# Optimization experiments

Measured on AMD Instinct MI355X. Metric: run time of the kernel, lower is better.

## Reference

```python
import jax, jax.numpy as jnp
import numpy as np

B, T, D, Uh = 64, 512, 1024, 1024

def _uniform(key, shape, scale=0.05):
    return jax.random.uniform(key, shape, dtype=jnp.float32, minval=-scale, maxval=scale)

def setup_inputs() -> dict:
    key = jax.random.key(0)
    ks = jax.random.split(key, 15)
    inp = {"x": jax.random.normal(ks[0], (B, T, D), dtype=jnp.float32)}
    names = ["fw", "fu", "fb", "iw", "iu", "ib", "cw", "cu", "cb", "ow", "ou", "ob"]
    shapes = [(D, Uh), (Uh, Uh), (Uh,)] * 4
    for n, s, k in zip(names, shapes, ks[1:13]):
        inp[n] = _uniform(k, s)
    inp["h0"] = _uniform(ks[13], (1, Uh))
    return inp

def reference(x, fw, fu, fb, iw, iu, ib, cw, cu, cb, ow, ou, ob, h0):
    # Concatenate the 4 gate weight matrices along the output dim: (D, 4U), (U, 4U), (4U,)
    W = jnp.concatenate([fw, iw, cw, ow], axis=1)
    Umat = jnp.concatenate([fu, iu, cu, ou], axis=1)
    b = jnp.concatenate([fb, ib, cb, ob], axis=0)
    # Input-to-gate projections for all timesteps at once: (B, T, 4U)
    xw = jnp.einsum('btd,dg->btg', x, W) + b
    h_init = jnp.repeat(h0, x.shape[0], axis=0)  # (B, U)

    def step(h, xw_t):
        g = xw_t + h @ Umat  # (B, 4U)
        f, i, c, o = jnp.split(g, 4, axis=-1)
        h1 = jax.nn.sigmoid(f) * h + jax.nn.sigmoid(i) * jnp.tanh(c)
        y1 = jax.nn.sigmoid(o) * jnp.tanh(h1)
        return h1, y1

    _, ys = jax.lax.scan(step, h_init, jnp.swapaxes(xw, 0, 1))  # ys: (T, B, U)
    return jnp.swapaxes(ys, 0, 1)  # (B, T, U)
```

## Files before the change

kernel.cpp:

```cpp
#include <hip/hip_runtime.h>
#include <hip/hip_bf16.h>

#define BB 64
#define TT 512
#define DD 1024
#define UU 1024

typedef __attribute__((ext_vector_type(8))) short short8;
typedef __attribute__((ext_vector_type(4))) float f32x4;
typedef unsigned long long ull;

static __device__ __forceinline__ unsigned short f2bf(float f) {
    unsigned int u = __float_as_uint(f);
    unsigned int r = (u + 0x7fffu + ((u >> 16) & 1u)) >> 16;
    return (unsigned short)r;
}
static __device__ __forceinline__ float bf2f(unsigned short s) {
    return __uint_as_float(((unsigned int)s) << 16);
}
static __device__ __forceinline__ float fsig(float x) {
    return 1.0f / (1.0f + __expf(-x));
}
static __device__ __forceinline__ float ftanh(float x) {
    float e = __expf(-2.0f * fabsf(x));
    float r = (1.0f - e) / (1.0f + e);
    return __builtin_copysignf(r, x);
}

__global__ __launch_bounds__(256) void pack_w(
    const float* __restrict__ w0, const float* __restrict__ w1,
    const float* __restrict__ w2, const float* __restrict__ w3,
    short* __restrict__ out)
{
    int tid = blockIdx.x * 256 + threadIdx.x;
    int lane = tid & 63;
    int kb = (tid >> 6) & 31;
    int n16 = tid >> 11;
    int col = (n16 << 4) + (lane & 15);
    int g = col >> 10, u = col & 1023;
    const float* __restrict__ src = (g == 0) ? w0 : (g == 1) ? w1 : (g == 2) ? w2 : w3;
    int kbase = kb * 32 + ((lane >> 4) << 3);
    short8 p;
#pragma unroll
    for (int i = 0; i < 8; ++i) p[i] = (short)f2bf(src[(size_t)(kbase + i) * UU + u]);
    *reinterpret_cast<short8*>(out + (size_t)tid * 8) = p;
}

__global__ __launch_bounds__(256) void init_hbf(const float* __restrict__ h0,
                                                unsigned short* __restrict__ hb)
{
    int i = blockIdx.x * 256 + threadIdx.x;
    hb[i] = f2bf(h0[i & (UU - 1)]);
}

__global__ __launch_bounds__(256) void gemm_xw(
    const float* __restrict__ x, const short* __restrict__ wpk,
    const float* __restrict__ fb, const float* __restrict__ ib,
    const float* __restrict__ cb, const float* __restrict__ ob,
    unsigned short* __restrict__ xw)
{
    __shared__ short As[128 * 40];
    __shared__ short Bs[8 * 512];

    const int tid = threadIdx.x;
    const int lane = tid & 63;
    const int wid = tid >> 6;
    const int wr = wid >> 1, wc = wid & 1;
    const int n0 = blockIdx.x << 7;
    const int m0 = blockIdx.y << 7;
    const int n16b = n0 >> 4;

    const int srow = tid >> 1;
    const int kh = tid & 1;
    const float* __restrict__ xrow = x + (size_t)(m0 + srow) * DD + kh * 16;
    const short* __restrict__ wsrc =
        wpk + ((size_t)(n16b + (tid >> 5)) * 32) * 512 + (size_t)(tid & 31) * 16;

    f32x4 acc[4][4];
#pragma unroll
    for (int i = 0; i < 4; ++i)
#pragma unroll
        for (int j = 0; j < 4; ++j) acc[i][j] = (f32x4){0.f, 0.f, 0.f, 0.f};

    const int aoff = (wr * 64 + (lane & 15)) * 40 + (lane >> 4) * 8;
    const int boff = (wc * 4) * 512 + lane * 8;

    for (int kb = 0; kb < 32; ++kb) {
        const float4* xp = reinterpret_cast<const float4*>(xrow + kb * 32);
        float4 v0 = xp[0], v1 = xp[1], v2 = xp[2], v3 = xp[3];
        short8 p0, p1;
        p0[0] = (short)f2bf(v0.x); p0[1] = (short)f2bf(v0.y);
        p0[2] = (short)f2bf(v0.z); p0[3] = (short)f2bf(v0.w);
        p0[4] = (short)f2bf(v1.x); p0[5] = (short)f2bf(v1.y);
        p0[6] = (short)f2bf(v1.z); p0[7] = (short)f2bf(v1.w);
        p1[0] = (short)f2bf(v2.x); p1[1] = (short)f2bf(v2.y);
        p1[2] = (short)f2bf(v2.z); p1[3] = (short)f2bf(v2.w);
        p1[4] = (short)f2bf(v3.x); p1[5] = (short)f2bf(v3.y);
        p1[6] = (short)f2bf(v3.z); p1[7] = (short)f2bf(v3.w);
        *reinterpret_cast<short8*>(&As[srow * 40 + kh * 16]) = p0;
        *reinterpret_cast<short8*>(&As[srow * 40 + kh * 16 + 8]) = p1;

        const short8* ws8 = reinterpret_cast<const short8*>(wsrc + (size_t)kb * 512);
        short8 b0v = ws8[0], b1v = ws8[1];
        *reinterpret_cast<short8*>(&Bs[tid * 16]) = b0v;
        *reinterpret_cast<short8*>(&Bs[tid * 16 + 8]) = b1v;
        __syncthreads();

        short8 af[4], bfr[4];
#pragma unroll
        for (int fi = 0; fi < 4; ++fi)
            af[fi] = *reinterpret_cast<const short8*>(&As[aoff + fi * 640]);
#pragma unroll
        for (int fj = 0; fj < 4; ++fj)
            bfr[fj] = *reinterpret_cast<const short8*>(&Bs[boff + fj * 512]);
#pragma unroll
        for (int fi = 0; fi < 4; ++fi)
#pragma unroll
            for (int fj = 0; fj < 4; ++fj)
                acc[fi][fj] = __builtin_amdgcn_mfma_f32_16x16x32_bf16(
                    af[fi], bfr[fj], acc[fi][fj], 0, 0, 0);
        __syncthreads();
    }

    const int g = n0 >> 10;
    const float* __restrict__ bias = (g == 0) ? fb : (g == 1) ? ib : (g == 2) ? cb : ob;
#pragma unroll
    for (int fi = 0; fi < 4; ++fi) {
#pragma unroll
        for (int fj = 0; fj < 4; ++fj) {
            int n = n0 + wc * 64 + fj * 16 + (lane & 15);
            int uc = n & 1023;
            int ub = uc >> 4, ul = uc & 15;
            float bv = bias[uc];
#pragma unroll
            for (int r = 0; r < 4; ++r) {
                int row = m0 + wr * 64 + fi * 16 + (lane >> 4) * 4 + r;
                int b = row >> 9, t = row & 511;
                float v = acc[fi][fj][r] + bv;
                size_t off = (((size_t)t * 64 + ub) * BB + b) * 64 + g * 16 + ul;
                xw[off] = f2bf(v);
            }
        }
    }
}

#define PHASE(MZ, R0, HLS, GBUF, HOWN, OMZ, OHLS, DO_POLL, POLL_T)                 \
  do {                                                                             \
    const unsigned short* __restrict__ xp =                                        \
        xw + ((size_t)t * 64 + ub) * 4096 + (size_t)((R0) + trow) * 64 + tcol;     \
    float xv0 = bf2f(xp[0]);                                                       \
    float xv1 = bf2f(xp[16]);                                                      \
    float xv2 = bf2f(xp[32]);                                                      \
    float xv3 = bf2f(xp[48]);                                                      \
    f32x4 acc0 = (f32x4){0.f, 0.f, 0.f, 0.f};                                      \
    f32x4 acc1 = (f32x4){0.f, 0.f, 0.f, 0.f};                                      \
    _Pragma("unroll")                                                              \
    for (int kg = 0; kg < 32; kg += 2) {                                           \
      short8 a0 = *reinterpret_cast<const short8*>(&HLS[aoff + kg * 32]);          \
      short8 a1 = *reinterpret_cast<const short8*>(&HLS[aoff + kg * 32 + 32]);     \
      acc0 = __builtin_amdgcn_mfma_f32_16x16x32_bf16(a0, bfr[kg], acc0, 0, 0, 0);  \
      acc1 = __builtin_amdgcn_mfma_f32_16x16x32_bf16(a1, bfr[kg + 1], acc1,        \
                                                     0, 0, 0);                     \
    }                                                                              \
    acc0[0] += acc1[0]; acc0[1] += acc1[1];                                        \
    acc0[2] += acc1[2]; acc0[3] += acc1[3];                                        \
    _Pragma("unroll")                                                              \
    for (int r = 0; r < 4; ++r)                                                    \
      GBUF[gi][(lane >> 4) * 4 + r][lane & 15] = acc0[r];                          \
    if (gi == 1 && (DO_POLL)) {                                                    \
      const int* fl = flg + ((size_t)(POLL_T) * 4 + (OMZ)) * 64 + lane;            \
      int v;                                                                       \
      do {                                                                         \
        v = __hip_atomic_load(fl, __ATOMIC_RELAXED, __HIP_MEMORY_SCOPE_AGENT);     \
        if (v == 0) __builtin_amdgcn_s_sleep(1);                                   \
      } while (v == 0);                                                            \
      asm volatile("" ::: "memory");                                               \
      const unsigned short* hc = hrot + (size_t)(POLL_T) * (BB * UU)               \
                                 + ((size_t)(OMZ) << 4) * UU + (size_t)(v - 1);    \
      _Pragma("unroll")                                                            \
      for (int p = 0; p < 32; ++p) {                                               \
        int row = p >> 1, half = p & 1;                                            \
        __builtin_amdgcn_global_load_lds(                                          \
            (const void*)(hc + (size_t)row * 1024 + half * 512 + (size_t)lane * 8),\
            (void*)&OHLS[row * 1032 + half * 512], 16, 0, 16);                     \
      }                                                                            \
    }                                                                              \
    asm volatile("s_waitcnt lgkmcnt(0)" ::: "memory");                             \
    __builtin_amdgcn_s_barrier();                                                  \
    asm volatile("" ::: "memory");                                                 \
    {                                                                              \
      float gf  = GBUF[0][trow][tcol] + xv0;                                       \
      float gii = GBUF[1][trow][tcol] + xv1;                                       \
      float gc  = GBUF[2][trow][tcol] + xv2;                                       \
      float go  = GBUF[3][trow][tcol] + xv3;                                       \
      float h1  = fsig(gf) * (HOWN) + fsig(gii) * ftanh(gc);                       \
      (HOWN) = h1;                                                                 \
      y[((size_t)((R0) + trow) * TT + t) * UU + u0 + tcol] = fsig(go) * ftanh(h1); \
      unsigned int hb16 = f2bf(h1);                                                \
      unsigned int n1 = __shfl_down(hb16, 1);                                      \
      unsigned int n2 = __shfl_down(hb16, 2);                                      \
      unsigned int n3 = __shfl_down(hb16, 3);                                      \
      if (t < TT - 1 && (lane & 3) == 0) {                                         \
        unsigned long long pv =                                                    \
            (unsigned long long)(hb16 | (n1 << 16)) |                              \
            ((unsigned long long)(n2 | (n3 << 16)) << 32);                         \
        unsigned short* dst = hrot + (size_t)(t + 1) * (BB * UU)                   \
                              + (size_t)((R0) + trow) * UU + u0 + tcol;            \
        __hip_atomic_store(reinterpret_cast<ull*>(dst), pv,                        \
                           __ATOMIC_RELAXED, __HIP_MEMORY_SCOPE_AGENT);            \
      }                                                                            \
    }                                                                              \
    __syncthreads();               \
    if (t < TT - 1 && gi == 0 && lane == 0)                                        \
      __hip_atomic_store(flg + ((size_t)(t + 1) * 4 + (MZ)) * 64 + ub, 1,          \
                         __ATOMIC_RELAXED, __HIP_MEMORY_SCOPE_AGENT);              \
  } while (0)

__global__ __launch_bounds__(256, 1) void lstm_scan(
    const unsigned short* __restrict__ xw, const float* __restrict__ h0,
    unsigned short* __restrict__ hrot,
    const short* __restrict__ upk,
    float* __restrict__ y, int* __restrict__ flg)
{
    __shared__ unsigned short hlsA[16 * 1032 + 8];
    __shared__ unsigned short hlsB[16 * 1032 + 8];
    __shared__ float gbufA[4][16][20];
    __shared__ float gbufB[4][16][20];

    const int tid = threadIdx.x;
    const int lane = tid & 63;
    const int gi = tid >> 6;
    const int z  = blockIdx.x >> 6;
    const int ub = blockIdx.x & 63;
    const int mzA = z * 2, mzB = z * 2 + 1;
    const int r0A = mzA << 4, r0B = mzB << 4;
    const int u0 = ub << 4;

    const short* __restrict__ bsrc =
        upk + ((size_t)(gi * 64 + ub) * 32) * 512 + (size_t)lane * 8;
    short8 bfr[32];
#pragma unroll
    for (int kb = 0; kb < 32; ++kb)
        bfr[kb] = *reinterpret_cast<const short8*>(bsrc + (size_t)kb * 512);

    const int aoff = (lane & 15) * 1032 + (lane >> 4) * 8;
    const int trow = tid >> 4, tcol = tid & 15;

    float h_ownA = h0[u0 + tcol];
    float h_ownB = h_ownA;

    if (gi == 1) {
#pragma unroll
        for (int p = 0; p < 32; ++p) {
            int row = p >> 1, half = p & 1;
            __builtin_amdgcn_global_load_lds(
                (const void*)(hrot + (size_t)r0A * UU + (size_t)row * 1024
                              + half * 512 + (size_t)lane * 8),
                (void*)&hlsA[row * 1032 + half * 512], 16, 0, 16);
            __builtin_amdgcn_global_load_lds(
                (const void*)(hrot + (size_t)r0B * UU + (size_t)row * 1024
                              + half * 512 + (size_t)lane * 8),
                (void*)&hlsB[row * 1032 + half * 512], 16, 0, 16);
        }
    }
    __syncthreads();

    for (int t = 0; t < TT; ++t) {
        PHASE(mzA, r0A, hlsA, gbufA, h_ownA, mzB, hlsB, (t >= 1), t);
        PHASE(mzB, r0B, hlsB, gbufB, h_ownB, mzA, hlsA, (t + 1 < TT), t + 1);
    }
}

extern "C" void kernel_launch(void* const* d_in, const int* in_sizes, int n_in,
                              void* d_out, int out_size, void* d_ws, size_t ws_size,
                              hipStream_t stream)
{
    const float* x  = (const float*)d_in[0];
    const float* fw = (const float*)d_in[1];
    const float* fu = (const float*)d_in[2];
    const float* fb = (const float*)d_in[3];
    const float* iw = (const float*)d_in[4];
    const float* iu = (const float*)d_in[5];
    const float* ib = (const float*)d_in[6];
    const float* cw = (const float*)d_in[7];
    const float* cu = (const float*)d_in[8];
    const float* cb = (const float*)d_in[9];
    const float* ow = (const float*)d_in[10];
    const float* ou = (const float*)d_in[11];
    const float* ob = (const float*)d_in[12];
    const float* h0 = (const float*)d_in[13];
    float* y = (float*)d_out;

    const size_t xw_elems = (size_t)TT * BB * 4 * UU;
    const size_t pk_elems = (size_t)4 * 1024 * 1024;
    const size_t hrot_elems = (size_t)(TT + 1) * BB * UU;

    char* wsb = (char*)d_ws;
    unsigned short* xw = (unsigned short*)wsb;
    short* upk = (short*)(wsb + xw_elems * 2);
    short* wpk = upk + pk_elems;
    unsigned short* hrot = (unsigned short*)(wpk + pk_elems);
    int* flg = (int*)(hrot + hrot_elems);

    pack_w<<<2048, 256, 0, stream>>>(fu, iu, cu, ou, upk);
    pack_w<<<2048, 256, 0, stream>>>(fw, iw, cw, ow, wpk);
    init_hbf<<<256, 256, 0, stream>>>(h0, hrot);
    gemm_xw<<<dim3(32, 256), 256, 0, stream>>>(x, wpk, fb, ib, cb, ob, xw);
    hipMemsetAsync(flg, 0, (size_t)(TT + 1) * 4 * 64 * sizeof(int), stream);

    lstm_scan<<<128, 256, 0, stream>>>(xw, h0, hrot, upk, y, flg);
}
```

Baseline: 2.444 ms.

## Replace block-wide syncthreads plus flag with per-wave byte flags and deferred publication

Each of the four waves now publishes its own byte of a 4-byte readiness flag after its vmcnt drains. The flag is set at the start of the next phase rather than after a full __syncthreads, and the poller waits for all four bytes (0x01010101). The y store moves after the h store so the h writes complete first, and the trailing __syncthreads becomes a raw s_barrier with a partial vmcnt wait. The aim is to take the block-wide drain and barrier off the critical path of the cross-block recurrence. The cost is more subtle memory-ordering reasoning, and it now writes hrot for the last timestep.

```diff
diff --git a/kernel.cpp b/kernel.cpp
--- a/kernel.cpp
+++ b/kernel.cpp
@@ -144,8 +144,15 @@
     }
 }
 
-#define PHASE(MZ, R0, HLS, GBUF, HOWN, OMZ, OHLS, DO_POLL, POLL_T)                 \
+#define PHASE(MZ, R0, HLS, GBUF, HOWN, OMZ, OHLS, DO_POLL, POLL_T, DO_FLAG, F_MZ, F_T) \
   do {                                                                             \
+    if (DO_FLAG) {                                                                 \
+      asm volatile("s_waitcnt vmcnt(0)" ::: "memory");                             \
+      if (lane == 0)                                                               \
+        __hip_atomic_store(                                                        \
+            (unsigned char*)flg + ((((size_t)(F_T)) * 4 + (F_MZ)) * 64 + ub) * 4 + gi, \
+            (unsigned char)1, __ATOMIC_RELAXED, __HIP_MEMORY_SCOPE_AGENT);         \
+    }                                                                              \
     const unsigned short* __restrict__ xp =                                        \
         xw + ((size_t)t * 64 + ub) * 4096 + (size_t)((R0) + trow) * 64 + tcol;     \
     float xv0 = bf2f(xp[0]);                                                       \
@@ -168,15 +175,17 @@
     for (int r = 0; r < 4; ++r)                                                    \
       GBUF[gi][(lane >> 4) * 4 + r][lane & 15] = acc0[r];                          \
     if (gi == 1 && (DO_POLL)) {                                                    \
-      const int* fl = flg + ((size_t)(POLL_T) * 4 + (OMZ)) * 64 + lane;            \
-      int v;                                                                       \
+      const unsigned int* fl =                                                     \
+          (const unsigned int*)flg + ((size_t)(POLL_T) * 4 + (OMZ)) * 64 + lane;   \
+      unsigned int v;                                                              \
       do {                                                                         \
         v = __hip_atomic_load(fl, __ATOMIC_RELAXED, __HIP_MEMORY_SCOPE_AGENT);     \
-        if (v == 0) __builtin_amdgcn_s_sleep(1);                                   \
-      } while (v == 0);                                                            \
+        if (v != 0x01010101u) __builtin_amdgcn_s_sleep(1);                         \
+      } while (v != 0x01010101u);                                                  \
       asm volatile("" ::: "memory");                                               \
       const unsigned short* hc = hrot + (size_t)(POLL_T) * (BB * UU)               \
-                                 + ((size_t)(OMZ) << 4) * UU + (size_t)(v - 1);    \
+                                 + ((size_t)(OMZ) << 4) * UU                       \
+                                 + (size_t)(v - 0x01010101u);                      \
       _Pragma("unroll")                                                            \
       for (int p = 0; p < 32; ++p) {                                               \
         int row = p >> 1, half = p & 1;                                            \
@@ -195,12 +204,11 @@
       float go  = GBUF[3][trow][tcol] + xv3;                                       \
       float h1  = fsig(gf) * (HOWN) + fsig(gii) * ftanh(gc);                       \
       (HOWN) = h1;                                                                 \
-      y[((size_t)((R0) + trow) * TT + t) * UU + u0 + tcol] = fsig(go) * ftanh(h1); \
       unsigned int hb16 = f2bf(h1);                                                \
       unsigned int n1 = __shfl_down(hb16, 1);                                      \
       unsigned int n2 = __shfl_down(hb16, 2);                                      \
       unsigned int n3 = __shfl_down(hb16, 3);                                      \
-      if (t < TT - 1 && (lane & 3) == 0) {                                         \
+      if ((lane & 3) == 0) {        \
         unsigned long long pv =                                                    \
             (unsigned long long)(hb16 | (n1 << 16)) |                              \
             ((unsigned long long)(n2 | (n3 << 16)) << 32);                         \
@@ -209,18 +217,19 @@
         __hip_atomic_store(reinterpret_cast<ull*>(dst), pv,                        \
                            __ATOMIC_RELAXED, __HIP_MEMORY_SCOPE_AGENT);            \
       }                                                                            \
+      y[((size_t)((R0) + trow) * TT + t) * UU + u0 + tcol] = fsig(go) * ftanh(h1); \
     }                                                                              \
-    __syncthreads();               \
-    if (t < TT - 1 && gi == 0 && lane == 0)                                        \
-      __hip_atomic_store(flg + ((size_t)(t + 1) * 4 + (MZ)) * 64 + ub, 1,          \
-                         __ATOMIC_RELAXED, __HIP_MEMORY_SCOPE_AGENT);              \
+    if (gi == 1 && (DO_POLL))                                                      \
+      asm volatile("s_waitcnt vmcnt(2)" ::: "memory");  \
+    __builtin_amdgcn_s_barrier();                                                  \
+    asm volatile("" ::: "memory");                                                 \
   } while (0)
 
 __global__ __launch_bounds__(256, 1) void lstm_scan(
     const unsigned short* __restrict__ xw, const float* __restrict__ h0,
     unsigned short* __restrict__ hrot,
     const short* __restrict__ upk,
-    float* __restrict__ y, int* __restrict__ flg)
+    float* __restrict__ y, unsigned int* __restrict__ flg)
 {
     __shared__ unsigned short hlsA[16 * 1032 + 8];
     __shared__ unsigned short hlsB[16 * 1032 + 8];
@@ -266,8 +275,10 @@
     __syncthreads();
 
     for (int t = 0; t < TT; ++t) {
-        PHASE(mzA, r0A, hlsA, gbufA, h_ownA, mzB, hlsB, (t >= 1), t);
-        PHASE(mzB, r0B, hlsB, gbufB, h_ownB, mzA, hlsA, (t + 1 < TT), t + 1);
+        PHASE(mzA, r0A, hlsA, gbufA, h_ownA, mzB, hlsB, (t >= 1), t,
+              (t >= 1), mzB, t);
+        PHASE(mzB, r0B, hlsB, gbufB, h_ownB, mzA, hlsA, (t + 1 < TT), t + 1,
+              1, mzA, t + 1);
     }
 }
 
@@ -300,13 +311,13 @@
     short* upk = (short*)(wsb + xw_elems * 2);
     short* wpk = upk + pk_elems;
     unsigned short* hrot = (unsigned short*)(wpk + pk_elems);
-    int* flg = (int*)(hrot + hrot_elems);
+    unsigned int* flg = (unsigned int*)(hrot + hrot_elems);
 
     pack_w<<<2048, 256, 0, stream>>>(fu, iu, cu, ou, upk);
     pack_w<<<2048, 256, 0, stream>>>(fw, iw, cw, ow, wpk);
     init_hbf<<<256, 256, 0, stream>>>(h0, hrot);
     gemm_xw<<<dim3(32, 256), 256, 0, stream>>>(x, wpk, fb, ib, cb, ob, xw);
-    hipMemsetAsync(flg, 0, (size_t)(TT + 1) * 4 * 64 * sizeof(int), stream);
+    hipMemsetAsync(flg, 0, (size_t)(TT + 1) * 4 * 64 * sizeof(unsigned int), stream);
 
     lstm_scan<<<128, 256, 0, stream>>>(xw, h0, hrot, upk, y, flg);
 }
```

Measured after the change: 5.440 ms. +122.6%, slower.

## Pre-convert x to bf16 and stream GEMM tiles via global_load_lds with swizzle

Applied to the files above, without the earlier changes.

Adds a separate kernel that converts x to bf16 once, so the input-projection GEMM reads half as many bytes and no longer converts each tile inline. The GEMM then fills its shared-memory tiles with direct global-to-LDS loads and an XOR swizzle that replaces the padded layout to avoid bank conflicts. This costs an extra full pass over x and a scratch buffer placed inside the hrot region, which is written later by the scan.

```diff
diff --git a/kernel.cpp b/kernel.cpp
--- a/kernel.cpp
+++ b/kernel.cpp
@@ -53,13 +53,27 @@
     hb[i] = f2bf(h0[i & (UU - 1)]);
 }
 
+__global__ __launch_bounds__(256) void cvt_x(const float* __restrict__ x,
+                                             unsigned short* __restrict__ xb)
+{
+    size_t i = ((size_t)blockIdx.x * 256 + threadIdx.x) * 8;
+    float4 v0 = *reinterpret_cast<const float4*>(x + i);
+    float4 v1 = *reinterpret_cast<const float4*>(x + i + 4);
+    short8 p;
+    p[0] = (short)f2bf(v0.x); p[1] = (short)f2bf(v0.y);
+    p[2] = (short)f2bf(v0.z); p[3] = (short)f2bf(v0.w);
+    p[4] = (short)f2bf(v1.x); p[5] = (short)f2bf(v1.y);
+    p[6] = (short)f2bf(v1.z); p[7] = (short)f2bf(v1.w);
+    *reinterpret_cast<short8*>(xb + i) = p;
+}
+
 __global__ __launch_bounds__(256) void gemm_xw(
-    const float* __restrict__ x, const short* __restrict__ wpk,
+    const unsigned short* __restrict__ xb, const short* __restrict__ wpk,
     const float* __restrict__ fb, const float* __restrict__ ib,
     const float* __restrict__ cb, const float* __restrict__ ob,
     unsigned short* __restrict__ xw)
 {
-    __shared__ short As[128 * 40];
+    __shared__ short As2[128 * 32];
     __shared__ short Bs[8 * 512];
 
     const int tid = threadIdx.x;
@@ -70,46 +84,37 @@
     const int m0 = blockIdx.y << 7;
     const int n16b = n0 >> 4;
 
-    const int srow = tid >> 1;
-    const int kh = tid & 1;
-    const float* __restrict__ xrow = x + (size_t)(m0 + srow) * DD + kh * 16;
-    const short* __restrict__ wsrc =
-        wpk + ((size_t)(n16b + (tid >> 5)) * 32) * 512 + (size_t)(tid & 31) * 16;
-
     f32x4 acc[4][4];
 #pragma unroll
     for (int i = 0; i < 4; ++i)
 #pragma unroll
         for (int j = 0; j < 4; ++j) acc[i][j] = (f32x4){0.f, 0.f, 0.f, 0.f};
 
-    const int aoff = (wr * 64 + (lane & 15)) * 40 + (lane >> 4) * 8;
+    const int aoff = (wr * 64 + (lane & 15)) * 32 + (((lane >> 4) ^ (lane & 3)) << 3);
     const int boff = (wc * 4) * 512 + lane * 8;
 
+    const int c0 = wid << 1;
+
     for (int kb = 0; kb < 32; ++kb) {
-        const float4* xp = reinterpret_cast<const float4*>(xrow + kb * 32);
-        float4 v0 = xp[0], v1 = xp[1], v2 = xp[2], v3 = xp[3];
-        short8 p0, p1;
-        p0[0] = (short)f2bf(v0.x); p0[1] = (short)f2bf(v0.y);
-        p0[2] = (short)f2bf(v0.z); p0[3] = (short)f2bf(v0.w);
-        p0[4] = (short)f2bf(v1.x); p0[5] = (short)f2bf(v1.y);
-        p0[6] = (short)f2bf(v1.z); p0[7] = (short)f2bf(v1.w);
-        p1[0] = (short)f2bf(v2.x); p1[1] = (short)f2bf(v2.y);
-        p1[2] = (short)f2bf(v2.z); p1[3] = (short)f2bf(v2.w);
-        p1[4] = (short)f2bf(v3.x); p1[5] = (short)f2bf(v3.y);
-        p1[6] = (short)f2bf(v3.z); p1[7] = (short)f2bf(v3.w);
-        *reinterpret_cast<short8*>(&As[srow * 40 + kh * 16]) = p0;
-        *reinterpret_cast<short8*>(&As[srow * 40 + kh * 16 + 8]) = p1;
-
-        const short8* ws8 = reinterpret_cast<const short8*>(wsrc + (size_t)kb * 512);
-        short8 b0v = ws8[0], b1v = ws8[1];
-        *reinterpret_cast<short8*>(&Bs[tid * 16]) = b0v;
-        *reinterpret_cast<short8*>(&Bs[tid * 16 + 8]) = b1v;
+#pragma unroll
+        for (int j = 0; j < 2; ++j) {
+            int c = c0 + j;
+            int row = (c << 4) + (lane >> 2);
+            int g = (lane & 3) ^ (row & 3);
+            __builtin_amdgcn_global_load_lds(
+                (const void*)(xb + (size_t)(m0 + row) * DD + kb * 32 + g * 8),
+                (void*)&As2[c * 512], 16, 0, 0);
+            __builtin_amdgcn_global_load_lds(
+                (const void*)(wpk + ((size_t)(n16b + c) * 32 + kb) * 512 + (size_t)lane * 8),
+                (void*)&Bs[c * 512], 16, 0, 0);
+        }
+        asm volatile("s_waitcnt vmcnt(0)" ::: "memory");
         __syncthreads();
 
         short8 af[4], bfr[4];
 #pragma unroll
         for (int fi = 0; fi < 4; ++fi)
-            af[fi] = *reinterpret_cast<const short8*>(&As[aoff + fi * 640]);
+            af[fi] = *reinterpret_cast<const short8*>(&As2[aoff + fi * 512]);
 #pragma unroll
         for (int fj = 0; fj < 4; ++fj)
             bfr[fj] = *reinterpret_cast<const short8*>(&Bs[boff + fj * 512]);
@@ -302,10 +307,13 @@
     unsigned short* hrot = (unsigned short*)(wpk + pk_elems);
     int* flg = (int*)(hrot + hrot_elems);
 
+    unsigned short* xb = hrot + (size_t)BB * UU;
+
     pack_w<<<2048, 256, 0, stream>>>(fu, iu, cu, ou, upk);
     pack_w<<<2048, 256, 0, stream>>>(fw, iw, cw, ow, wpk);
     init_hbf<<<256, 256, 0, stream>>>(h0, hrot);
-    gemm_xw<<<dim3(32, 256), 256, 0, stream>>>(x, wpk, fb, ib, cb, ob, xw);
+    cvt_x<<<16384, 256, 0, stream>>>(x, xb);
+    gemm_xw<<<dim3(32, 256), 256, 0, stream>>>(xb, wpk, fb, ib, cb, ob, xw);
     hipMemsetAsync(flg, 0, (size_t)(TT + 1) * 4 * 64 * sizeof(int), stream);
 
     lstm_scan<<<128, 256, 0, stream>>>(xw, h0, hrot, upk, y, flg);
```

Measured after the change: 2.235 ms. 1.09x faster.
